# Kernel tuning notes

Measured on AMD Instinct MI355X. Metric: run time of the kernel, lower is better.

## Reference

```python
import jax, jax.numpy as jnp
import numpy as np

N = 1_000_000
HID = 128

def setup_inputs() -> dict:
    key = jax.random.key(0)
    ks = jax.random.split(key, 4)
    F = jnp.eye(2, dtype=jnp.float32)[None] + 0.1 * jax.random.normal(ks[0], (N, 2, 2), dtype=jnp.float32)
    W1 = jax.random.normal(ks[1], (7, HID), dtype=jnp.float32) * (1.0 / np.sqrt(7))
    b1 = jnp.zeros((HID,), dtype=jnp.float32)
    W2 = jax.random.normal(ks[2], (HID, HID), dtype=jnp.float32) * (1.0 / np.sqrt(HID))
    b2 = jnp.zeros((HID,), dtype=jnp.float32)
    W3 = jax.random.normal(ks[3], (HID, 4), dtype=jnp.float32) * (1.0 / np.sqrt(HID))
    b3 = jnp.zeros((4,), dtype=jnp.float32)
    return {"F": F, "W1": W1, "b1": b1, "W2": W2, "b2": b2, "W3": W3, "b3": b3}

def reference(F, W1, b1, W2, b2, W3, b3):
    F = F.reshape(-1, 2, 2)                      # [N,2,2]
    U, sigma, Vh = jnp.linalg.svd(F)             # batched 2x2 SVD
    R = jnp.matmul(U, Vh)                        # rotation part, [N,2,2]
    FtF = jnp.einsum('nij,nik->njk', F, F)       # F^T F, [N,2,2]
    I = jnp.eye(2, dtype=F.dtype)
    I1 = sigma - 1.0                             # [N,2]
    I2 = (FtF - I).reshape(-1, 4)                # [N,4]
    det = F[:, 0, 0] * F[:, 1, 1] - F[:, 0, 1] * F[:, 1, 0]
    I3 = det[:, None] - 1.0                      # [N,1]
    inv = jnp.concatenate([I1, I2, I3], axis=1)  # [N,7]
    h = jax.nn.relu(inv @ W1 + b1)
    h = jax.nn.relu(h @ W2 + b2)
    x = (h @ W3 + b3).reshape(-1, 2, 2)
    x = (x + jnp.swapaxes(x, 1, 2)) * 0.5        # symmetrize
    delta_Fp = jnp.matmul(R, x)
    return delta_Fp + F
```

## Files before the change

### kernel.cpp

```cpp
#include <hip/hip_runtime.h>

typedef _Float16 f16x8 __attribute__((ext_vector_type(8)));
typedef __fp16   fp16x2r __attribute__((ext_vector_type(2)));
typedef float    f32x4 __attribute__((ext_vector_type(4)));

#define MFMA(a, b, c) __builtin_amdgcn_mfma_f32_16x16x32_f16((a), (b), (c), 0, 0, 0)

__device__ inline f16x8 zero8() {
    f16x8 z;
#pragma unroll
    for (int i = 0; i < 8; ++i) z[i] = (_Float16)0.0f;
    return z;
}

__device__ inline f16x8 relu_pack8_rtn(f32x4 lo, f32x4 hi) {
    f16x8 v;
#pragma unroll
    for (int i = 0; i < 4; ++i) {
        v[i]     = (_Float16)fmaxf(lo[i], 0.f);
        v[i + 4] = (_Float16)fmaxf(hi[i], 0.f);
    }
    return v;
}

__device__ inline f16x8 relu_pack8_rtz(f32x4 lo, f32x4 hi) {
    const fp16x2r p0 = __builtin_amdgcn_cvt_pkrtz(fmaxf(lo[0], 0.f), fmaxf(lo[1], 0.f));
    const fp16x2r p1 = __builtin_amdgcn_cvt_pkrtz(fmaxf(lo[2], 0.f), fmaxf(lo[3], 0.f));
    const fp16x2r p2 = __builtin_amdgcn_cvt_pkrtz(fmaxf(hi[0], 0.f), fmaxf(hi[1], 0.f));
    const fp16x2r p3 = __builtin_amdgcn_cvt_pkrtz(fmaxf(hi[2], 0.f), fmaxf(hi[3], 0.f));
    uint4 u = { __builtin_bit_cast(unsigned int, p0), __builtin_bit_cast(unsigned int, p1),
                __builtin_bit_cast(unsigned int, p2), __builtin_bit_cast(unsigned int, p3) };
    return __builtin_bit_cast(f16x8, u);
}

__global__ __launch_bounds__(256, 1)
void DeformationCorrector_78967268704761_kernel(
        const float* __restrict__ F,
        const float* __restrict__ W1, const float* __restrict__ b1,
        const float* __restrict__ W2, const float* __restrict__ b2,
        const float* __restrict__ W3, const float* __restrict__ b3,
        float* __restrict__ out, int N)
{
    __shared__ __align__(16) _Float16 W2A[8][4][64][8];
    __shared__ __align__(16) _Float16 W1A[8][16][8];
    __shared__ __align__(16) _Float16 W3A[4][16][8];
    __shared__ __align__(16) float    b2L[128];
    __shared__ __align__(16) float    b3L[4];
    __shared__ __align__(16) _Float16 invL[4][64][8];

    const int tid  = threadIdx.x;
    const int lane = tid & 63;
    const int w    = tid >> 6;
    const int l15  = tid & 15;
    const int quad = (tid >> 4) & 3;

    for (int m = tid; m < 128 * 128; m += 256) {
        const int k = m >> 7, n = m & 127;
        const int s = k >> 5, j = ((k >> 4) & 1) * 4 + (k & 3), q = (k >> 2) & 3;
        W2A[n >> 4][s][q * 16 + (n & 15)][j] = (_Float16)W2[m];
    }
    for (int f = tid; f < 1024; f += 256) {
        const int mt = f >> 7, n15 = (f >> 3) & 15, j = f & 7;
        W1A[mt][n15][j] = (_Float16)((j < 7) ? W1[j * 128 + mt * 16 + n15]
                                             : b1[mt * 16 + n15]);
    }
    for (int f = tid; f < 512; f += 256) {
        const int s3 = f >> 7, idx = (f >> 3) & 15, j = f & 7;
        const int q = idx >> 2, c3 = idx & 3;
        const int ch2 = (2 * s3 + (j >> 2)) * 16 + q * 4 + (j & 3);
        W3A[s3][idx][j] = (_Float16)W3[ch2 * 4 + c3];
    }
    if (tid < 128) b2L[tid] = b2[tid];
    if (tid < 4)   b3L[tid] = b3[tid];
    __syncthreads();

    const int ntiles = (N + 255) >> 8;
    const int stride = (int)gridDim.x;

    for (int tile = blockIdx.x; tile < ntiles; tile += stride) {
        const int p = tile * 256 + tid;

        float a, b, c, d;
        if (p < N) {
            const float4 f4 = *(const float4*)(F + 4ll * p);
            a = f4.x; b = f4.y; c = f4.z; d = f4.w;
        } else { a = 1.f; b = 0.f; c = 0.f; d = 1.f; }

        const float x1 = a + d, y1 = c - b, x2 = a - d, y2 = c + b;
        const float h1v = sqrtf(x1 * x1 + y1 * y1);
        const float h2v = sqrtf(x2 * x2 + y2 * y2);
        const float s1 = 0.5f * (h1v + h2v), s2 = 0.5f * (h1v - h2v);
        const float ir = 1.0f / h1v;
        const float Rc = x1 * ir, Rs = y1 * ir;
        f16x8 iv;
        iv[0] = (_Float16)(s1 - 1.f);
        iv[1] = (_Float16)(s2 - 1.f);
        iv[2] = (_Float16)(a * a + c * c - 1.f);
        const float i3 = a * b + c * d;
        iv[3] = (_Float16)i3;
        iv[4] = (_Float16)i3;
        iv[5] = (_Float16)(b * b + d * d - 1.f);
        iv[6] = (_Float16)(a * d - b * c - 1.f);
        iv[7] = (_Float16)1.0f;
        *(f16x8*)(&invL[w][lane][0]) = iv;

#pragma unroll 1
        for (int q4 = 0; q4 < 4; ++q4) {
            const f16x8 B1 = (quad == 0)
                ? *(const f16x8*)(&invL[w][q4 * 16 + l15][0]) : zero8();

            f16x8 B2[4];
#pragma unroll
            for (int s = 0; s < 4; ++s) {
                const f16x8 aLo = (quad == 0) ? *(const f16x8*)(&W1A[2 * s][l15][0])     : zero8();
                const f16x8 aHi = (quad == 0) ? *(const f16x8*)(&W1A[2 * s + 1][l15][0]) : zero8();
                const f32x4 cz  = {0.f, 0.f, 0.f, 0.f};
                const f32x4 dLo = MFMA(aLo, B1, cz);
                const f32x4 dHi = MFMA(aHi, B1, cz);
                B2[s] = relu_pack8_rtn(dLo, dHi);
            }

            f32x4 acc3 = {0.f, 0.f, 0.f, 0.f};
#pragma unroll
            for (int s3 = 0; s3 < 4; ++s3) {
                f32x4 accE = *(const f32x4*)(&b2L[(2 * s3) * 16 + quad * 4]);
                f32x4 accO = *(const f32x4*)(&b2L[(2 * s3 + 1) * 16 + quad * 4]);
#pragma unroll
                for (int s = 0; s < 4; ++s) {
                    const f16x8 aE = *(const f16x8*)(&W2A[2 * s3][s][lane][0]);
                    const f16x8 aO = *(const f16x8*)(&W2A[2 * s3 + 1][s][lane][0]);
                    accE = MFMA(aE, B2[s], accE);
                    accO = MFMA(aO, B2[s], accO);
                }
                const f16x8 a3 = (l15 < 4) ? *(const f16x8*)(&W3A[s3][quad * 4 + l15][0]) : zero8();
                const f16x8 b3f = relu_pack8_rtz(accE, accO);
                acc3 = MFMA(a3, b3f, acc3);
            }

            if (quad == 0) {
                const f32x4 b3v4 = *(const f32x4*)(&b3L[0]);
                *(f16x8*)(&invL[w][q4 * 16 + l15][0]) =
                    __builtin_bit_cast(f16x8, acc3 + b3v4);
            }
        }

        const f32x4 xv = __builtin_bit_cast(f32x4, *(const f16x8*)(&invL[w][lane][0]));
        const float xm  = 0.5f * (xv[1] + xv[2]);
        const float d00 = Rc * xv[0] - Rs * xm;
        const float d01 = Rc * xm    - Rs * xv[3];
        const float d10 = Rs * xv[0] + Rc * xm;
        const float d11 = Rs * xm    + Rc * xv[3];
        if (p < N) {
            float4 o;
            o.x = a + d00; o.y = b + d01; o.z = c + d10; o.w = d + d11;
            *(float4*)(out + 4ll * p) = o;
        }
    }
}

extern "C" void kernel_launch(void* const* d_in, const int* in_sizes, int n_in,
                              void* d_out, int out_size, void* d_ws, size_t ws_size,
                              hipStream_t stream) {
    const float* F  = (const float*)d_in[0];
    const float* W1 = (const float*)d_in[1];
    const float* b1 = (const float*)d_in[2];
    const float* W2 = (const float*)d_in[3];
    const float* b2 = (const float*)d_in[4];
    const float* W3 = (const float*)d_in[5];
    const float* b3 = (const float*)d_in[6];
    float* out = (float*)d_out;
    const int N = in_sizes[0] / 4;
    const int ntiles = (N + 255) / 256;
    const int grid = ntiles < 512 ? ntiles : 512;
    DeformationCorrector_78967268704761_kernel<<<grid, 256, 0, stream>>>(
        F, W1, b1, W2, b2, W3, b3, out, N);
}
```

Baseline: 133.7 us.

## Prefetch next tile's F and spill current F to LDS across MLP

Loads the next tile's F values at the top of each iteration so the global load latency overlaps with the MFMA-heavy MLP. To keep register pressure down, the current tile's F is stored to a per-lane LDS scratch and the rotation is recomputed from it after the MLP instead of being held live. The W1 fragment loads also drop the quad==0 select, since B1 is zero for the other quads anyway. In exchange it adds LDS traffic, one extra sqrt and reciprocal per element, and four extra live registers for the prefetched values.

```diff
diff --git a/kernel.cpp b/kernel.cpp
--- a/kernel.cpp
+++ b/kernel.cpp
@@ -47,6 +47,7 @@
     __shared__ __align__(16) float    b2L[128];
     __shared__ __align__(16) float    b3L[4];
     __shared__ __align__(16) _Float16 invL[4][64][8];
+    __shared__ __align__(16) float    Esc[4][64][4];
 
     const int tid  = threadIdx.x;
     const int lane = tid & 63;
@@ -77,32 +78,44 @@
     const int ntiles = (N + 255) >> 8;
     const int stride = (int)gridDim.x;
 
+    float a, b, c, d;
+    {
+        const int p0 = blockIdx.x * 256 + tid;
+        if (blockIdx.x < ntiles && p0 < N) {
+            const float4 f4 = *(const float4*)(F + 4ll * p0);
+            a = f4.x; b = f4.y; c = f4.z; d = f4.w;
+        } else { a = 1.f; b = 0.f; c = 0.f; d = 1.f; }
+    }
+
     for (int tile = blockIdx.x; tile < ntiles; tile += stride) {
+        float na = 1.f, nb = 0.f, nc = 0.f, nd = 1.f;
+        {
+            const int pn = (tile + stride) * 256 + tid;
+            if (tile + stride < ntiles && pn < N) {
+                const float4 f4 = *(const float4*)(F + 4ll * pn);
+                na = f4.x; nb = f4.y; nc = f4.z; nd = f4.w;
+            }
+        }
         const int p = tile * 256 + tid;
 
-        float a, b, c, d;
-        if (p < N) {
-            const float4 f4 = *(const float4*)(F + 4ll * p);
-            a = f4.x; b = f4.y; c = f4.z; d = f4.w;
-        } else { a = 1.f; b = 0.f; c = 0.f; d = 1.f; }
-
-        const float x1 = a + d, y1 = c - b, x2 = a - d, y2 = c + b;
-        const float h1v = sqrtf(x1 * x1 + y1 * y1);
-        const float h2v = sqrtf(x2 * x2 + y2 * y2);
-        const float s1 = 0.5f * (h1v + h2v), s2 = 0.5f * (h1v - h2v);
-        const float ir = 1.0f / h1v;
-        const float Rc = x1 * ir, Rs = y1 * ir;
-        f16x8 iv;
-        iv[0] = (_Float16)(s1 - 1.f);
-        iv[1] = (_Float16)(s2 - 1.f);
-        iv[2] = (_Float16)(a * a + c * c - 1.f);
-        const float i3 = a * b + c * d;
-        iv[3] = (_Float16)i3;
-        iv[4] = (_Float16)i3;
-        iv[5] = (_Float16)(b * b + d * d - 1.f);
-        iv[6] = (_Float16)(a * d - b * c - 1.f);
-        iv[7] = (_Float16)1.0f;
-        *(f16x8*)(&invL[w][lane][0]) = iv;
+        {
+            const float x1 = a + d, y1 = c - b, x2 = a - d, y2 = c + b;
+            const float h1v = sqrtf(x1 * x1 + y1 * y1);
+            const float h2v = sqrtf(x2 * x2 + y2 * y2);
+            const float s1 = 0.5f * (h1v + h2v), s2 = 0.5f * (h1v - h2v);
+            f16x8 iv;
+            iv[0] = (_Float16)(s1 - 1.f);
+            iv[1] = (_Float16)(s2 - 1.f);
+            iv[2] = (_Float16)(a * a + c * c - 1.f);
+            const float i3 = a * b + c * d;
+            iv[3] = (_Float16)i3;
+            iv[4] = (_Float16)i3;
+            iv[5] = (_Float16)(b * b + d * d - 1.f);
+            iv[6] = (_Float16)(a * d - b * c - 1.f);
+            iv[7] = (_Float16)1.0f;
+            *(f16x8*)(&invL[w][lane][0]) = iv;
+        }
+        *(f32x4*)(&Esc[w][lane][0]) = (f32x4){a, b, c, d};
 
 #pragma unroll 1
         for (int q4 = 0; q4 < 4; ++q4) {
@@ -112,8 +125,8 @@
             f16x8 B2[4];
 #pragma unroll
             for (int s = 0; s < 4; ++s) {
-                const f16x8 aLo = (quad == 0) ? *(const f16x8*)(&W1A[2 * s][l15][0])     : zero8();
-                const f16x8 aHi = (quad == 0) ? *(const f16x8*)(&W1A[2 * s + 1][l15][0]) : zero8();
+                const f16x8 aLo = *(const f16x8*)(&W1A[2 * s][l15][0]);
+                const f16x8 aHi = *(const f16x8*)(&W1A[2 * s + 1][l15][0]);
                 const f32x4 cz  = {0.f, 0.f, 0.f, 0.f};
                 const f32x4 dLo = MFMA(aLo, B1, cz);
                 const f32x4 dHi = MFMA(aHi, B1, cz);
@@ -144,6 +157,11 @@
             }
         }
 
+        const f32x4 fv = *(const f32x4*)(&Esc[w][lane][0]);
+        const float x1e = fv[0] + fv[3], y1e = fv[2] - fv[1];
+        const float h1e = sqrtf(x1e * x1e + y1e * y1e);
+        const float ire = 1.0f / h1e;
+        const float Rc = x1e * ire, Rs = y1e * ire;
         const f32x4 xv = __builtin_bit_cast(f32x4, *(const f16x8*)(&invL[w][lane][0]));
         const float xm  = 0.5f * (xv[1] + xv[2]);
         const float d00 = Rc * xv[0] - Rs * xm;
@@ -152,9 +170,11 @@
         const float d11 = Rs * xm    + Rc * xv[3];
         if (p < N) {
             float4 o;
-            o.x = a + d00; o.y = b + d01; o.z = c + d10; o.w = d + d11;
+            o.x = fv[0] + d00; o.y = fv[1] + d01; o.z = fv[2] + d10; o.w = fv[3] + d11;
             *(float4*)(out + 4ll * p) = o;
         }
+
+        a = na; b = nb; c = nc; d = nd;
     }
 }
 
```

Result: slower. 144.5 us (+8.0%).

## Stage W2 prologue load via async global_load_lds pipeline and drop W1 zero-masking

Applied to the files above, without the earlier changes.

Replaces the per-element strided global loads of W2 in the kernel prologue with a 4-deep pipeline of direct global-to-LDS 16-byte loads, staged into a new LDS buffer and then converted to fp16 and scattered into the MFMA layout. Waits are handled with manual vmcnt/lgkmcnt waitcnts so later chunks are fetched while earlier ones are converted. It also removes the quad==0 select on the W1 operand, relying on B1 already being zero for the other quads. This adds 32KB of LDS and fragile hand-placed waitcnts, and the prologue is only a small part of the total run time.

```diff
diff --git a/kernel.cpp b/kernel.cpp
--- a/kernel.cpp
+++ b/kernel.cpp
@@ -32,6 +32,17 @@
                 __builtin_bit_cast(unsigned int, p2), __builtin_bit_cast(unsigned int, p3) };
     return __builtin_bit_cast(f16x8, u);
 }
+
+__device__ inline void gload16(const float* g, float* l) {
+    __builtin_amdgcn_global_load_lds(
+        (const __attribute__((address_space(1))) void*)g,
+        (__attribute__((address_space(3))) void*)l, 16, 0, 0);
+}
+
+
+#define WAITVM(N)  asm volatile("s_waitcnt vmcnt(" #N ")" ::: "memory")
+#define WAITLGKM0  asm volatile("s_waitcnt lgkmcnt(0)" ::: "memory")
+#define MEMFENCE   asm volatile("" ::: "memory")
 
 __global__ __launch_bounds__(256, 1)
 void DeformationCorrector_78967268704761_kernel(
@@ -47,6 +58,7 @@
     __shared__ __align__(16) float    b2L[128];
     __shared__ __align__(16) float    b3L[4];
     __shared__ __align__(16) _Float16 invL[4][64][8];
+    __shared__ __align__(16) float    Wstg[4][2048];
 
     const int tid  = threadIdx.x;
     const int lane = tid & 63;
@@ -54,11 +66,6 @@
     const int l15  = tid & 15;
     const int quad = (tid >> 4) & 3;
 
-    for (int m = tid; m < 128 * 128; m += 256) {
-        const int k = m >> 7, n = m & 127;
-        const int s = k >> 5, j = ((k >> 4) & 1) * 4 + (k & 3), q = (k >> 2) & 3;
-        W2A[n >> 4][s][q * 16 + (n & 15)][j] = (_Float16)W2[m];
-    }
     for (int f = tid; f < 1024; f += 256) {
         const int mt = f >> 7, n15 = (f >> 3) & 15, j = f & 7;
         W1A[mt][n15][j] = (_Float16)((j < 7) ? W1[j * 128 + mt * 16 + n15]
@@ -72,6 +79,53 @@
     }
     if (tid < 128) b2L[tid] = b2[tid];
     if (tid < 4)   b3L[tid] = b3[tid];
+    MEMFENCE;
+
+#define ISSUE_CHUNK(k_, buf_) do {                                                    \
+        const float* gb = W2 + (k_) * 2048 + w * 64                                   \
+                             + (lane >> 4) * 256 + (lane & 15) * 4;                   \
+        gload16(gb,        &Wstg[(buf_)][w * 512]);                                   \
+        gload16(gb + 1024, &Wstg[(buf_)][w * 512 + 256]);                             \
+    } while (0)
+
+#define SCAT(c_, u_, val_) do {                                                       \
+        const int m = (c_) * 2048 + (u_) * 256 + tid;                                 \
+        const int k = m >> 7, n = m & 127;                                            \
+        const int s = k >> 5, j = ((k >> 4) & 1) * 4 + (k & 3), q = (k >> 2) & 3;     \
+        W2A[n >> 4][s][q * 16 + (n & 15)][j] = (_Float16)(val_);                      \
+    } while (0)
+
+#define PSTEP(c_, VMN_, DO_ISSUE_) do {                                               \
+        WAITVM(VMN_);                                                                 \
+        const float t0 = Wstg[(c_) & 3][w * 512 + 0 * 64 + lane];                     \
+        const float t1 = Wstg[(c_) & 3][w * 512 + 1 * 64 + lane];                     \
+        const float t2 = Wstg[(c_) & 3][w * 512 + 2 * 64 + lane];                     \
+        const float t3 = Wstg[(c_) & 3][w * 512 + 3 * 64 + lane];                     \
+        const float t4 = Wstg[(c_) & 3][w * 512 + 4 * 64 + lane];                     \
+        const float t5 = Wstg[(c_) & 3][w * 512 + 5 * 64 + lane];                     \
+        const float t6 = Wstg[(c_) & 3][w * 512 + 6 * 64 + lane];                     \
+        const float t7 = Wstg[(c_) & 3][w * 512 + 7 * 64 + lane];                     \
+        WAITLGKM0;                         \
+        if (DO_ISSUE_) ISSUE_CHUNK((c_) + 4, (c_) & 3);                               \
+        MEMFENCE;                                                                     \
+        SCAT(c_, 0, t0); SCAT(c_, 1, t1); SCAT(c_, 2, t2); SCAT(c_, 3, t3);           \
+        SCAT(c_, 4, t4); SCAT(c_, 5, t5); SCAT(c_, 6, t6); SCAT(c_, 7, t7);           \
+        MEMFENCE;                                                                     \
+    } while (0)
+
+    ISSUE_CHUNK(0, 0); ISSUE_CHUNK(1, 1); ISSUE_CHUNK(2, 2); ISSUE_CHUNK(3, 3);
+    MEMFENCE;
+    PSTEP(0, 6, 1);
+    PSTEP(1, 6, 1);
+    PSTEP(2, 6, 1);
+    PSTEP(3, 6, 1);
+    PSTEP(4, 6, 0);
+    PSTEP(5, 4, 0);
+    PSTEP(6, 2, 0);
+    PSTEP(7, 0, 0);
+#undef PSTEP
+#undef SCAT
+#undef ISSUE_CHUNK
     __syncthreads();
 
     const int ntiles = (N + 255) >> 8;
@@ -112,8 +166,8 @@
             f16x8 B2[4];
 #pragma unroll
             for (int s = 0; s < 4; ++s) {
-                const f16x8 aLo = (quad == 0) ? *(const f16x8*)(&W1A[2 * s][l15][0])     : zero8();
-                const f16x8 aHi = (quad == 0) ? *(const f16x8*)(&W1A[2 * s + 1][l15][0]) : zero8();
+                const f16x8 aLo = *(const f16x8*)(&W1A[2 * s][l15][0]);
+                const f16x8 aHi = *(const f16x8*)(&W1A[2 * s + 1][l15][0]);
                 const f32x4 cz  = {0.f, 0.f, 0.f, 0.f};
                 const f32x4 dLo = MFMA(aLo, B1, cz);
                 const f32x4 dHi = MFMA(aHi, B1, cz);
```

Result: slower. 139.3 us (+4.2%).
